# Kernel tuning notes

Measured on AMD Instinct MI355X. Metric: run time of the kernel, lower is better.

The kernel has to match this reference:

```python
import jax, jax.numpy as jnp
from jax import lax
import numpy as np

N = 2000      # num_nodes
T_IN = 24
T_OUT = 12
B = 32
H = 64        # hidden_dim
D = 10        # embed_dim / adapt_dim
K = 2         # cheb_k
C_IN = 1


def setup_inputs() -> dict:
    key = jax.random.key(0)
    ks = jax.random.split(key, 13)
    s = 0.1  # xavier-ish scale
    f32 = jnp.float32
    return {
        "x": jax.random.normal(ks[0], (B, T_IN, N), f32),
        "node_emb": jax.random.normal(ks[1], (N, D), f32) * s,
        "adapt_emb": jax.random.normal(ks[2], (N, D), f32) * s,
        # layer 0 NAPL weight/bias pools (gate: 2H out, candidate: H out)
        "Wg0": jax.random.normal(ks[3], (D, K, C_IN + H, 2 * H), f32) * s,
        "bg0": jax.random.normal(ks[4], (D, 2 * H), f32) * s,
        "Wc0": jax.random.normal(ks[5], (D, K, C_IN + H, H), f32) * s,
        "bc0": jax.random.normal(ks[6], (D, H), f32) * s,
        # layer 1 pools (input is hidden_dim)
        "Wg1": jax.random.normal(ks[7], (D, K, 2 * H, 2 * H), f32) * s,
        "bg1": jax.random.normal(ks[8], (D, 2 * H), f32) * s,
        "Wc1": jax.random.normal(ks[9], (D, K, 2 * H, H), f32) * s,
        "bc1": jax.random.normal(ks[10], (D, H), f32) * s,
        # 1x1 conv head == per-node linear hidden -> T_out
        "head_w": jax.random.normal(ks[11], (T_OUT, H), f32) * s,
        "head_b": jnp.zeros((T_OUT,), f32),
    }


def reference(x, node_emb, adapt_emb, Wg0, bg0, Wc0, bc0, Wg1, bg1, Wc1, bc1,
              head_w, head_b):
    Bn, T, Nn = x.shape
    # adaptive adjacency: row-softmax(relu(E E^T)); no prior -> A_used = A_adapt
    A = jax.nn.softmax(jax.nn.relu(adapt_emb @ adapt_emb.T), axis=-1)
    supports = jnp.stack([jnp.eye(Nn, dtype=x.dtype), A])  # (K, N, N)

    def napl(Wp, bp):
        # node-adaptive parameter learning: per-node weights/biases
        W = jnp.einsum('nd,dkio->nkio', node_emb, Wp)  # (N, K, Cin, Cout)
        b = node_emb @ bp                              # (N, Cout)
        return W, b

    p = [napl(Wg0, bg0), napl(Wc0, bc0), napl(Wg1, bg1), napl(Wc1, bc1)]

    def gconv(inp, W, b):
        # inp: (B, N, C)
        xg = jnp.einsum('knm,bmc->bknc', supports, inp)      # (B, K, N, C)
        return jnp.einsum('bkni,nkio->bno', xg, W) + b       # (B, N, Cout)

    def cell(xt, h, gW, gb, cW, cb):
        zr = jax.nn.sigmoid(gconv(jnp.concatenate([xt, h], -1), gW, gb))
        z, r = jnp.split(zr, 2, axis=-1)
        hc = jnp.tanh(gconv(jnp.concatenate([xt, r * h], -1), cW, cb))
        return z * h + (1.0 - z) * hc

    def step(carry, xt):
        h0, h1 = carry
        h0 = cell(xt, h0, p[0][0], p[0][1], p[1][0], p[1][1])
        h1 = cell(h0, h1, p[2][0], p[2][1], p[3][0], p[3][1])
        return (h0, h1), None

    xs = jnp.transpose(x[..., None], (1, 0, 2, 3))  # (T, B, N, 1)
    h0 = jnp.zeros((Bn, Nn, H), x.dtype)
    h1 = jnp.zeros((Bn, Nn, H), x.dtype)
    (h0, h1), _ = lax.scan(step, (h0, h1), xs)

    # 1x1 conv head on (B, H, N, 1) == per-node linear: (B, T_out, N)
    y = jnp.einsum('bnh,oh->bon', h1, head_w) + head_b[None, :, None]
    return y
```

## Files before the change

### kernel.cpp

```cpp
#include <hip/hip_runtime.h>
#include <math.h>

#define NN 2000
#define BB 32
#define TT 24
#define T_OUT 12
#define HH 64
#define DD 10
#define NP 2048
#define BC 2048

typedef unsigned short ushort_t;
typedef __bf16 bf16x8 __attribute__((ext_vector_type(8)));
typedef float f32x4 __attribute__((ext_vector_type(4)));

__device__ __forceinline__ float sigmoidf_(float x) { return 1.f / (1.f + expf(-x)); }

__device__ __forceinline__ ushort_t f2bf(float f) {
    unsigned int u = __float_as_uint(f);
    unsigned int r = (u + 0x7FFFu + ((u >> 16) & 1u)) >> 16;
    return (ushort_t)r;
}
__device__ __forceinline__ float bf2f(ushort_t s) {
    return __uint_as_float(((unsigned int)s) << 16);
}

__device__ __forceinline__ void glld16(const ushort_t* g, ushort_t* lds) {
    __builtin_amdgcn_global_load_lds(
        (const __attribute__((address_space(1))) char*)g,
        (__attribute__((address_space(3))) char*)lds, 16, 0, 0);
}

__device__ __forceinline__ unsigned lds_off(const void* p) {
    return (unsigned)(size_t)(__attribute__((address_space(3))) const char*)p;
}

constexpr size_t SZ_NPNP2 = (size_t)NP * NP * 2;
constexpr size_t SZ_ST4   = (size_t)NN * BC * 4;
constexpr size_t SZ_NPB2  = (size_t)NP * BC * 2;

constexpr size_t ABF_OFF  = 0;
constexpr size_t H0F_OFF  = ABF_OFF + SZ_NPNP2;
constexpr size_t H1F_OFF  = H0F_OFF + SZ_ST4;
constexpr size_t ZF_OFF   = H1F_OFF + SZ_ST4;
constexpr size_t H0B_OFF  = ZF_OFF + SZ_ST4;
constexpr size_t H1B_OFF  = H0B_OFF + SZ_NPB2;
constexpr size_t RHB_OFF  = H1B_OFF + SZ_NPB2;
constexpr size_t AH0_OFF  = RHB_OFF + SZ_NPB2;
constexpr size_t AHX_OFF  = AH0_OFF + SZ_NPB2;
constexpr size_t AXF_OFF  = AHX_OFF + SZ_NPB2;
constexpr size_t BTG0_OFF = AXF_OFF + (size_t)BB * TT * NN * 4;
constexpr size_t BTC0_OFF = BTG0_OFF + (size_t)DD * 128 * 128 * 2;
constexpr size_t BTG1_OFF = BTC0_OFF + (size_t)DD * 64 * 128 * 2;
constexpr size_t BTC1_OFF = BTG1_OFF + (size_t)DD * 128 * 256 * 2;
constexpr size_t WS_TOP   = BTC1_OFF + (size_t)DD * 64 * 256 * 2;
constexpr size_t ZF1_OFF  = WS_TOP;
constexpr size_t RHB1_OFF = ZF1_OFF + SZ_ST4;
constexpr size_t AHY_OFF  = RHB1_OFF + SZ_NPB2;
constexpr size_t TOP_PIPE = AHY_OFF + SZ_NPB2;
constexpr size_t H0B2_OFF = TOP_PIPE;
constexpr size_t TOP_PIPE2 = H0B2_OFF + SZ_NPB2;

__global__ __launch_bounds__(256) void compute_A_kernel(const float* __restrict__ E,
                                                        float* __restrict__ A) {
    const int row = blockIdx.x;
    const int tid = threadIdx.x;
    float er[DD];
#pragma unroll
    for (int d = 0; d < DD; ++d) er[d] = E[row * DD + d];
    __shared__ float red[8];

    float lmax = -1e30f;
    for (int c = tid; c < NN; c += 256) {
        float s = 0.f;
#pragma unroll
        for (int d = 0; d < DD; ++d) s += er[d] * E[c * DD + d];
        s = fmaxf(s, 0.f);
        A[(size_t)row * NN + c] = s;
        lmax = fmaxf(lmax, s);
    }
#pragma unroll
    for (int o = 32; o > 0; o >>= 1) lmax = fmaxf(lmax, __shfl_down(lmax, o, 64));
    if ((tid & 63) == 0) red[tid >> 6] = lmax;
    __syncthreads();
    const float rmax = fmaxf(fmaxf(red[0], red[1]), fmaxf(red[2], red[3]));
    __syncthreads();

    float lsum = 0.f;
    for (int c = tid; c < NN; c += 256) {
        float v = expf(A[(size_t)row * NN + c] - rmax);
        A[(size_t)row * NN + c] = v;
        lsum += v;
    }
#pragma unroll
    for (int o = 32; o > 0; o >>= 1) lsum += __shfl_down(lsum, o, 64);
    if ((tid & 63) == 0) red[4 + (tid >> 6)] = lsum;
    __syncthreads();
    const float inv = 1.f / (red[4] + red[5] + red[6] + red[7]);
    for (int c = tid; c < NN; c += 256) A[(size_t)row * NN + c] *= inv;
}

__global__ __launch_bounds__(256) void convert_A(const float* __restrict__ Af,
                                                 ushort_t* __restrict__ Ab) {
    size_t idx = (size_t)blockIdx.x * 256 + threadIdx.x;
    int r = (int)(idx >> 11), c = (int)(idx & 2047);
    float v = (r < NN && c < NN) ? Af[(size_t)r * NN + c] : 0.f;
    Ab[idx] = f2bf(v);
}

__global__ __launch_bounds__(256) void ax2_kernel(const float* __restrict__ A,
                                                  const float* __restrict__ x,
                                                  float* __restrict__ Ax) {
    __shared__ float As[64][66];
    __shared__ float xs[64][50];
    const int n0 = blockIdx.x * 64;
    const int b0 = blockIdx.y * 2;
    const int tid = threadIdx.x;
    const int tr = tid >> 4, tc = tid & 15;
    float acc[4][3] = {};

    for (int m0 = 0; m0 < NN; m0 += 64) {
#pragma unroll
        for (int l = 0; l < 16; ++l) {
            int idx = tid + l * 256;
            int mm = idx & 63, r = idx >> 6;
            int n = n0 + r, m = m0 + mm;
            As[mm][r] = (n < NN && m < NN) ? A[(size_t)n * NN + m] : 0.f;
        }
#pragma unroll
        for (int l = 0; l < 12; ++l) {
            int idx = tid + l * 256;
            int mm = idx & 63, col = idx >> 6;
            int m = m0 + mm;
            int bl = col / 24, t = col - bl * 24;
            xs[mm][col] = (m < NN) ? x[((size_t)(b0 + bl) * TT + t) * NN + m] : 0.f;
        }
        __syncthreads();
#pragma unroll 4
        for (int mm = 0; mm < 64; ++mm) {
            float2 a01 = *(const float2*)&As[mm][tr * 4];
            float2 a23 = *(const float2*)&As[mm][tr * 4 + 2];
            float xv[3];
            xv[0] = xs[mm][tc * 3];
            xv[1] = xs[mm][tc * 3 + 1];
            xv[2] = xs[mm][tc * 3 + 2];
            float av[4] = {a01.x, a01.y, a23.x, a23.y};
#pragma unroll
            for (int i = 0; i < 4; ++i)
#pragma unroll
                for (int j = 0; j < 3; ++j) acc[i][j] += av[i] * xv[j];
        }
        __syncthreads();
    }
#pragma unroll
    for (int i = 0; i < 4; ++i) {
        const int n = n0 + tr * 4 + i;
        if (n < NN) {
#pragma unroll
            for (int j = 0; j < 3; ++j) {
                int col = tc * 3 + j;
                int bl = col / 24, t = col - bl * 24;
                Ax[((size_t)(b0 + bl) * TT + t) * NN + n] = acc[i][j];
            }
        }
    }
}


__device__ __forceinline__ void gemm_body(int bx, int by,
                                          const ushort_t* __restrict__ Ab,
                                          const ushort_t* __restrict__ H,
                                          ushort_t* __restrict__ Y, char* smem) {
    ushort_t* As = (ushort_t*)smem;
    ushort_t* Bs = (ushort_t*)(smem + 16384);
    const int tid = threadIdx.x;
    const int w = tid >> 6, l = tid & 63, lr = l & 15, lg = l >> 4;
    const int n0 = bx * 128, j0 = by * 128;
    f32x4 acc[8][2] = {};

    const unsigned bs0 = lds_off(Bs);
    const unsigned btr_b[2] = {
        bs0 + 2u * ((unsigned)(w * 2 + 0) * 512 + (unsigned)lg * 128 + (unsigned)lr),
        bs0 + 2u * ((unsigned)(w * 2 + 1) * 512 + (unsigned)lg * 128 + (unsigned)lr)};

    for (int ks = 0; ks < NP / 64; ++ks) {
        const int k0 = ks * 64;
#pragma unroll
        for (int p = 0; p < 4; ++p) {
            const int idx = p * 256 + tid;
            const int row = idx >> 3, sl = idx & 7;
            glld16(Ab + (size_t)(n0 + row) * NP + k0 + ((sl ^ (row & 7)) << 3),
                   (ushort_t*)((char*)As + idx * 16));
        }
#pragma unroll
        for (int p = 0; p < 4; ++p) {
            const int idx = p * 256 + tid;
            const int g = idx >> 9, li = idx & 511;
            const int row = k0 + g * 32 + ((li >> 3) & 7) * 4 + ((li >> 1) & 3);
            const int col = j0 + (li >> 6) * 16 + (li & 1) * 8;
            glld16(H + (size_t)row * BC + col,
                   (ushort_t*)((char*)Bs + g * 8192 + li * 16));
        }
        __syncthreads();

        unsigned long long bq[2][2][2];
        asm volatile(
            "ds_read_b64_tr_b16 %0, %8 offset:0\n\t"
            "ds_read_b64_tr_b16 %1, %8 offset:128\n\t"
            "ds_read_b64_tr_b16 %2, %9 offset:0\n\t"
            "ds_read_b64_tr_b16 %3, %9 offset:128\n\t"
            "ds_read_b64_tr_b16 %4, %8 offset:8192\n\t"
            "ds_read_b64_tr_b16 %5, %8 offset:8320\n\t"
            "ds_read_b64_tr_b16 %6, %9 offset:8192\n\t"
            "ds_read_b64_tr_b16 %7, %9 offset:8320"
            : "=v"(bq[0][0][0]), "=v"(bq[0][0][1]), "=v"(bq[0][1][0]), "=v"(bq[0][1][1]),
              "=v"(bq[1][0][0]), "=v"(bq[1][0][1]), "=v"(bq[1][1][0]), "=v"(bq[1][1][1])
            : "v"(btr_b[0]), "v"(btr_b[1]));
        asm volatile("s_waitcnt lgkmcnt(0)" ::: "memory");
        __builtin_amdgcn_sched_barrier(0);
        bf16x8 bv[2][2];
#pragma unroll
        for (int kk = 0; kk < 2; ++kk)
#pragma unroll
            for (int nt = 0; nt < 2; ++nt) {
                union { unsigned long long q[2]; bf16x8 f; } u;
                u.q[0] = bq[kk][nt][0];
                u.q[1] = bq[kk][nt][1];
                bv[kk][nt] = u.f;
            }

#pragma unroll
        for (int kk = 0; kk < 2; ++kk)
#pragma unroll
            for (int m = 0; m < 8; ++m) {
                const int rr = m * 16 + lr;
                const bf16x8 av = *(const bf16x8*)&As[rr * 64 + (((kk * 4 + lg) ^ (rr & 7)) << 3)];
#pragma unroll
                for (int nt = 0; nt < 2; ++nt)
                    acc[m][nt] = __builtin_amdgcn_mfma_f32_16x16x32_bf16(av, bv[kk][nt], acc[m][nt], 0, 0, 0);
            }
        __syncthreads();
    }

#pragma unroll
    for (int m = 0; m < 8; ++m)
#pragma unroll
        for (int r = 0; r < 4; ++r) {
            const int n = n0 + m * 16 + lg * 4 + r;
            if (n < NN) {
#pragma unroll
                for (int nt = 0; nt < 2; ++nt)
                    Y[(size_t)n * BC + j0 + w * 32 + nt * 16 + lr] = f2bf(acc[m][nt][r]);
            }
        }
}

template <int NSEGS, int CO, bool GATE, bool HASX>
__device__ __forceinline__ void napl_body(
    int bid, char* smem,
    const ushort_t* __restrict__ Bt, const float* __restrict__ bp,
    const float* __restrict__ emb, const float* __restrict__ WxPool,
    const ushort_t* __restrict__ s0p, const ushort_t* __restrict__ s1p,
    const ushort_t* __restrict__ s2p, const ushort_t* __restrict__ s3p,
    const float* __restrict__ xv, const float* __restrict__ axv,
    const float* hf, float* __restrict__ zf,
    ushort_t* __restrict__ outb, float* outf, int t) {
    constexpr int K = NSEGS * 64;
    constexpr int NT = (CO == 128) ? 2 : 1;
    constexpr int NHALF = NSEGS / 2;
    ushort_t* As = (ushort_t*)smem;
    const int tid = threadIdx.x;
    const int w = tid >> 6, l = tid & 63, lr = l & 15, lg = l >> 4;
    const int n0 = bid * 2;
    const int ob = w * (16 * NT);
    const ushort_t* segs[4] = {s0p, s1p, s2p, s3p};

#pragma unroll
    for (int s = 0; s < NSEGS; ++s) {
        const ushort_t* sp = segs[s];
#pragma unroll
        for (int p = 0; p < 2; ++p) {
            const int idx = p * 256 + tid;
            const int row = idx >> 3, c16 = idx & 7;
            glld16(sp + (size_t)(n0 + (row >> 5)) * BC + (row & 31) * 64 +
                       ((c16 ^ (row & 7)) << 3),
                   (ushort_t*)((char*)As + s * 8192 + idx * 16));
        }
    }
    __syncthreads();

    f32x4 OUT[4][NT] = {};
#pragma unroll 1
    for (int hf2 = 0; hf2 < NHALF; ++hf2) {
        bf16x8 av[4][4];
#pragma unroll
        for (int c = 0; c < 4; ++c) {
            const int s = hf2 * 2 + (c >> 1);
            const int kin = (c & 1) * 32 + lg * 8;
#pragma unroll
            for (int m = 0; m < 4; ++m) {
                const int rr = m * 16 + lr;
                av[c][m] = *(const bf16x8*)&As[s * 4096 + rr * 64 + (kin ^ ((rr & 7) << 3))];
            }
        }
#pragma unroll 1
        for (int d = 0; d < DD; ++d) {
            const ushort_t* btd = Bt + (size_t)d * CO * K;
            const float ea = emb[n0 * DD + d];
            const float eb = emb[(n0 + 1) * DD + d];
            f32x4 P[4][NT] = {};
#pragma unroll
            for (int c = 0; c < 4; ++c) {
                const int kg = (hf2 * 2 + (c >> 1)) * 64 + (c & 1) * 32 + lg * 8;
                bf16x8 bv[NT];
#pragma unroll
                for (int nt = 0; nt < NT; ++nt)
                    bv[nt] = *(const bf16x8*)&btd[(size_t)(ob + nt * 16 + lr) * K + kg];
#pragma unroll
                for (int m = 0; m < 4; ++m)
#pragma unroll
                    for (int nt = 0; nt < NT; ++nt)
                        P[m][nt] = __builtin_amdgcn_mfma_f32_16x16x32_bf16(av[c][m], bv[nt], P[m][nt], 0, 0, 0);
            }
#pragma unroll
            for (int m = 0; m < 4; ++m) {
                const float e = (m < 2) ? ea : eb;
#pragma unroll
                for (int nt = 0; nt < NT; ++nt)
#pragma unroll
                    for (int r = 0; r < 4; ++r)
                        OUT[m][nt][r] += e * P[m][nt][r];
            }
        }
    }

    float bias[2][NT];
#pragma unroll
    for (int nd = 0; nd < 2; ++nd)
#pragma unroll
        for (int nt = 0; nt < NT; ++nt) {
            float s_ = 0.f;
#pragma unroll
            for (int d = 0; d < DD; ++d)
                s_ += emb[(n0 + nd) * DD + d] * bp[d * CO + ob + nt * 16 + lr];
            bias[nd][nt] = s_;
        }
    float wx[2][2][NT] = {};
    if (HASX) {
#pragma unroll
        for (int kk = 0; kk < 2; ++kk)
#pragma unroll
            for (int nd = 0; nd < 2; ++nd)
#pragma unroll
                for (int nt = 0; nt < NT; ++nt) {
                    float s_ = 0.f;
#pragma unroll
                    for (int d = 0; d < DD; ++d)
                        s_ += emb[(n0 + nd) * DD + d] *
                              WxPool[(size_t)(d * 2 + kk) * 65 * CO + ob + nt * 16 + lr];
                    wx[kk][nd][nt] = s_;
                }
    }

#pragma unroll
    for (int m = 0; m < 4; ++m) {
        const int nd = m >> 1;
        const int n = n0 + nd;
#pragma unroll
        for (int r = 0; r < 4; ++r) {
            const int row = m * 16 + lg * 4 + r;
            const int b = row & 31;
            const size_t nb = (size_t)n * BC + b * 64;
            float xt = 0.f, axt = 0.f;
            if (HASX) {
                xt = xv[((size_t)b * TT + t) * NN + n];
                axt = axv[((size_t)b * TT + t) * NN + n];
            }
#pragma unroll
            for (int nt = 0; nt < NT; ++nt) {
                const int o = ob + nt * 16 + lr;
                float val = OUT[m][nt][r] + bias[nd][nt];
                if (HASX) val += xt * wx[0][nd][nt] + axt * wx[1][nd][nt];
                if (GATE) {
                    const float sg = sigmoidf_(val);
                    if (ob < 64) {
                        zf[nb + o] = sg;
                    } else {
                        outb[nb + (o - 64)] = f2bf(sg * hf[nb + (o - 64)]);
                    }
                } else {
                    const float hc = tanhf(val);
                    const float z = zf[nb + o];
                    const float hn = z * hf[nb + o] + (1.f - z) * hc;
                    outf[nb + o] = hn;
                    outb[nb + o] = f2bf(hn);
                }
            }
        }
    }
}


__global__ __launch_bounds__(256) void gemm_trb(const ushort_t* __restrict__ Ab,
                                                const ushort_t* __restrict__ H0,
                                                ushort_t* __restrict__ Y0,
                                                const ushort_t* __restrict__ H1,
                                                ushort_t* __restrict__ Y1) {
    __shared__ __align__(16) char smem[32768];
    gemm_body(blockIdx.x, blockIdx.y, Ab,
              (blockIdx.z == 0) ? H0 : H1, (blockIdx.z == 0) ? Y0 : Y1, smem);
}

template <int NSEGS, int CO, bool GATE, bool HASX>
__global__ __launch_bounds__(256) void napl2(
    const ushort_t* __restrict__ Bt, const float* __restrict__ bp,
    const float* __restrict__ emb, const float* __restrict__ WxPool,
    const ushort_t* __restrict__ s0p, const ushort_t* __restrict__ s1p,
    const ushort_t* __restrict__ s2p, const ushort_t* __restrict__ s3p,
    const float* __restrict__ xv, const float* __restrict__ axv,
    const float* hf, float* __restrict__ zf,
    ushort_t* __restrict__ outb, float* outf, int t) {
    __shared__ __align__(16) char smem[NSEGS * 8192];
    napl_body<NSEGS, CO, GATE, HASX>(blockIdx.x, smem, Bt, bp, emb, WxPool,
                                     s0p, s1p, s2p, s3p, xv, axv, hf, zf, outb, outf, t);
}

__global__ __launch_bounds__(256) void mergeA_k(
    const ushort_t* __restrict__ Abf, const ushort_t* __restrict__ Hg,
    ushort_t* __restrict__ Yg,
    const ushort_t* __restrict__ Bt, const float* __restrict__ bp,
    const float* __restrict__ emb, const float* __restrict__ Wx,
    const ushort_t* __restrict__ s0, const ushort_t* __restrict__ s1,
    const float* __restrict__ xv, const float* __restrict__ axv,
    const float* hf, float* __restrict__ zf, ushort_t* __restrict__ outb, int t) {
    __shared__ __align__(16) char smem[32768];
    const int g = blockIdx.x;
    if (g < 256)
        gemm_body(g & 15, g >> 4, Abf, Hg, Yg, smem);
    else
        napl_body<2, 128, true, true>(g - 256, smem, Bt, bp, emb, Wx,
                                      s0, s1, s0, s0, xv, axv, hf, zf, outb, nullptr, t);
}

__global__ __launch_bounds__(256) void mergeB_k(
    const ushort_t* __restrict__ Abf, const ushort_t* __restrict__ Hg,
    ushort_t* __restrict__ Yg,
    const ushort_t* __restrict__ Bt, const float* __restrict__ bp,
    const float* __restrict__ emb,
    const ushort_t* __restrict__ s0, const ushort_t* __restrict__ s1,
    const ushort_t* __restrict__ s2, const ushort_t* __restrict__ s3,
    const float* hf, float* __restrict__ zf,
    ushort_t* __restrict__ outb, float* outf, int t) {
    __shared__ __align__(16) char smem[32768];
    const int g = blockIdx.x;
    if (g < 256)
        gemm_body(g & 15, g >> 4, Abf, Hg, Yg, smem);
    else
        napl_body<4, 64, false, false>(g - 256, smem, Bt, bp, emb, nullptr,
                                       s0, s1, s2, s3, nullptr, nullptr, hf, zf, outb, outf, t);
}

__global__ __launch_bounds__(256) void mergeC_k(
    const ushort_t* __restrict__ Abf, const ushort_t* __restrict__ Hg,
    ushort_t* __restrict__ Yg,
    const ushort_t* __restrict__ Bt, const float* __restrict__ bp,
    const float* __restrict__ emb, const float* __restrict__ Wx,
    const ushort_t* __restrict__ s0, const ushort_t* __restrict__ s1,
    const float* __restrict__ xv, const float* __restrict__ axv,
    const float* hf, float* __restrict__ zf,
    ushort_t* __restrict__ outb, float* outf, int t) {
    __shared__ __align__(16) char smem[32768];
    const int g = blockIdx.x;
    if (g < 256)
        gemm_body(g & 15, g >> 4, Abf, Hg, Yg, smem);
    else
        napl_body<2, 64, false, true>(g - 256, smem, Bt, bp, emb, Wx,
                                      s0, s1, s0, s0, xv, axv, hf, zf, outb, outf, t);
}

__global__ __launch_bounds__(256) void mergeG_k(
    const ushort_t* __restrict__ Btg1, const float* __restrict__ bg1,
    const ushort_t* __restrict__ Btg0, const float* __restrict__ bg0,
    const float* __restrict__ emb, const float* __restrict__ Wg0,
    const ushort_t* __restrict__ hbt, const ushort_t* __restrict__ Ah0,
    const ushort_t* __restrict__ h1b, const ushort_t* __restrict__ AhX,
    const float* __restrict__ xv, const float* __restrict__ axv,
    const float* h0f, const float* h1f,
    float* __restrict__ zf0, float* __restrict__ zf1,
    ushort_t* __restrict__ rhb0, ushort_t* __restrict__ rhb1, int t) {
    __shared__ __align__(16) char smem[32768];
    const int g = blockIdx.x;
    if (g < 1000)
        napl_body<4, 128, true, false>(g, smem, Btg1, bg1, emb, nullptr,
                                       hbt, Ah0, h1b, AhX, nullptr, nullptr,
                                       h1f, zf1, rhb1, nullptr, t);
    else
        napl_body<2, 128, true, true>(g - 1000, smem, Btg0, bg0, emb, Wg0,
                                      hbt, Ah0, hbt, hbt, xv, axv,
                                      h0f, zf0, rhb0, nullptr, t + 1);
}

__global__ __launch_bounds__(256) void mergeCC_k(
    const ushort_t* __restrict__ Btc1, const float* __restrict__ bc1,
    const ushort_t* __restrict__ Btc0, const float* __restrict__ bc0,
    const float* __restrict__ emb, const float* __restrict__ Wc0,
    const ushort_t* __restrict__ hbt, ushort_t* __restrict__ hbt1,
    const ushort_t* __restrict__ Ah0, const ushort_t* __restrict__ rhb1,
    const ushort_t* __restrict__ AhX, const ushort_t* __restrict__ AhY,
    const ushort_t* __restrict__ rhb0,
    const float* __restrict__ xv, const float* __restrict__ axv,
    float* h0f, float* h1f,
    float* __restrict__ zf0, float* __restrict__ zf1,
    ushort_t* __restrict__ h1b, int t) {
    __shared__ __align__(16) char smem[32768];
    const int g = blockIdx.x;
    if (g < 1000)
        napl_body<4, 64, false, false>(g, smem, Btc1, bc1, emb, nullptr,
                                       hbt, Ah0, rhb1, AhX, nullptr, nullptr,
                                       h1f, zf1, h1b, h1f, t);
    else
        napl_body<2, 64, false, true>(g - 1000, smem, Btc0, bc0, emb, Wc0,
                                      rhb0, AhY, rhb0, rhb0, xv, axv,
                                      h0f, zf0, hbt1, h0f, t + 1);
}

template <int CI, int CO, bool L0>
__global__ __launch_bounds__(256) void prepW(const float* __restrict__ Wp,
                                             ushort_t* __restrict__ Bt) {
    constexpr int K = L0 ? 128 : 256;
    const int idx = blockIdx.x * 256 + threadIdx.x;
    if (idx >= DD * CO * K) return;
    const int d = idx / (CO * K);
    const int rem = idx - d * CO * K;
    const int o = rem / K;
    const int k = rem - o * K;
    const int s = k >> 6, c = k & 63;
    const int kk = L0 ? s : (s & 1);
    const int i = L0 ? (1 + c) : ((s >> 1) * 64 + c);
    Bt[idx] = f2bf(Wp[((size_t)(d * 2 + kk) * CI + i) * CO + o]);
}

__global__ __launch_bounds__(256) void head_kernel(const float* __restrict__ h1,
                                                   const float* __restrict__ hw,
                                                   const float* __restrict__ hb,
                                                   float* __restrict__ y) {
    __shared__ float wl[T_OUT * HH];
    const int tid = threadIdx.x;
    for (int idx = tid; idx < T_OUT * HH; idx += 256) wl[idx] = hw[idx];
    __syncthreads();
    const int gi = blockIdx.x * 256 + tid;
    if (gi >= BB * NN) return;
    const int b = gi / NN, n = gi % NN;
    float acc[T_OUT];
#pragma unroll
    for (int ot = 0; ot < T_OUT; ++ot) acc[ot] = hb[ot];
    for (int h = 0; h < HH; ++h) {
        float v = h1[(size_t)n * BC + b * 64 + h];
#pragma unroll
        for (int ot = 0; ot < T_OUT; ++ot) acc[ot] += v * wl[ot * HH + h];
    }
#pragma unroll
    for (int ot = 0; ot < T_OUT; ++ot)
        y[((size_t)b * T_OUT + ot) * NN + n] = acc[ot];
}

extern "C" void kernel_launch(void* const* d_in, const int* in_sizes, int n_in,
                              void* d_out, int out_size, void* d_ws, size_t ws_size,
                              hipStream_t stream) {
    const float* x = (const float*)d_in[0];
    const float* node_emb = (const float*)d_in[1];
    const float* adapt_emb = (const float*)d_in[2];
    const float* Wg0 = (const float*)d_in[3];
    const float* bg0 = (const float*)d_in[4];
    const float* Wc0 = (const float*)d_in[5];
    const float* bc0 = (const float*)d_in[6];
    const float* Wg1 = (const float*)d_in[7];
    const float* bg1 = (const float*)d_in[8];
    const float* Wc1 = (const float*)d_in[9];
    const float* bc1 = (const float*)d_in[10];
    const float* head_w = (const float*)d_in[11];
    const float* head_b = (const float*)d_in[12];
    float* y = (float*)d_out;

    char* ws = (char*)d_ws;
    ushort_t* Abf  = (ushort_t*)(ws + ABF_OFF);
    float* h0f = (float*)(ws + H0F_OFF);
    float* h1f = (float*)(ws + H1F_OFF);
    float* zf  = (float*)(ws + ZF_OFF);
    ushort_t* h0b = (ushort_t*)(ws + H0B_OFF);
    ushort_t* h1b = (ushort_t*)(ws + H1B_OFF);
    ushort_t* rhb = (ushort_t*)(ws + RHB_OFF);
    ushort_t* Ah0 = (ushort_t*)(ws + AH0_OFF);
    ushort_t* AhX = (ushort_t*)(ws + AHX_OFF);
    float* Axf = (float*)(ws + AXF_OFF);
    ushort_t* Btg0 = (ushort_t*)(ws + BTG0_OFF);
    ushort_t* Btc0 = (ushort_t*)(ws + BTC0_OFF);
    ushort_t* Btg1 = (ushort_t*)(ws + BTG1_OFF);
    ushort_t* Btc1 = (ushort_t*)(ws + BTC1_OFF);
    float* Af32 = zf;

    const bool pipe2 = (ws_size >= TOP_PIPE2);
    const bool pipe = (ws_size >= TOP_PIPE);

    hipMemsetAsync(h0f, 0, SZ_ST4, stream);
    hipMemsetAsync(h1f, 0, SZ_ST4, stream);
    hipMemsetAsync(h0b, 0, SZ_NPB2, stream);
    hipMemsetAsync(h1b, 0, SZ_NPB2, stream);
    hipMemsetAsync(rhb, 0, SZ_NPB2, stream);
    hipMemsetAsync(Ah0, 0, SZ_NPB2, stream);
    hipMemsetAsync(AhX, 0, SZ_NPB2, stream);

    compute_A_kernel<<<NN, 256, 0, stream>>>(adapt_emb, Af32);
    ax2_kernel<<<dim3(32, 16), 256, 0, stream>>>(Af32, x, Axf);
    convert_A<<<(NP * NP) / 256, 256, 0, stream>>>(Af32, Abf);
    prepW<65, 128, true><<<(DD * 128 * 128 + 255) / 256, 256, 0, stream>>>(Wg0, Btg0);
    prepW<65, 64, true><<<(DD * 64 * 128 + 255) / 256, 256, 0, stream>>>(Wc0, Btc0);
    prepW<128, 128, false><<<(DD * 128 * 256 + 255) / 256, 256, 0, stream>>>(Wg1, Btg1);
    prepW<128, 64, false><<<(DD * 64 * 256 + 255) / 256, 256, 0, stream>>>(Wc1, Btc1);

    const dim3 gG1(NP / 128, NP / 128, 1);
    const dim3 gG2(NP / 128, NP / 128, 2);
    const int gN = NN * BB / 64;

    if (pipe2) {
        float* zf0 = zf;
        ushort_t* rhb0 = rhb;
        float* zf1 = (float*)(ws + ZF1_OFF);
        ushort_t* rhb1 = (ushort_t*)(ws + RHB1_OFF);
        ushort_t* AhY = (ushort_t*)(ws + AHY_OFF);
        ushort_t* h0b2 = (ushort_t*)(ws + H0B2_OFF);
        hipMemsetAsync(rhb1, 0, SZ_NPB2, stream);
        hipMemsetAsync(h0b2, 0, SZ_NPB2, stream);
        ushort_t* hb[2] = {h0b, h0b2};

        napl2<2, 128, true, true><<<gN, 256, 0, stream>>>(
            Btg0, bg0, node_emb, Wg0, h0b, Ah0, h0b, h0b, x, Axf, h0f, zf0, rhb0, nullptr, 0);
        gemm_trb<<<gG1, 256, 0, stream>>>(Abf, rhb0, AhY, rhb0, AhY);
        napl2<2, 64, false, true><<<gN, 256, 0, stream>>>(
            Btc0, bc0, node_emb, Wc0, rhb0, AhY, rhb0, rhb0, x, Axf, h0f, zf0, hb[0], h0f, 0);
        gemm_trb<<<gG1, 256, 0, stream>>>(Abf, hb[0], Ah0, hb[0], Ah0);

        for (int t = 0; t < TT - 1; ++t) {
            ushort_t* hbt = hb[t & 1];
            ushort_t* hbt1 = hb[(t + 1) & 1];
            mergeG_k<<<2000, 256, 0, stream>>>(Btg1, bg1, Btg0, bg0, node_emb, Wg0,
                hbt, Ah0, h1b, AhX, x, Axf, h0f, h1f, zf0, zf1, rhb0, rhb1, t);
            gemm_trb<<<gG2, 256, 0, stream>>>(Abf, rhb1, AhX, rhb0, AhY);
            mergeCC_k<<<2000, 256, 0, stream>>>(Btc1, bc1, Btc0, bc0, node_emb, Wc0,
                hbt, hbt1, Ah0, rhb1, AhX, AhY, rhb0, x, Axf, h0f, h1f, zf0, zf1, h1b, t);
            gemm_trb<<<gG2, 256, 0, stream>>>(Abf, h1b, AhX, hbt1, Ah0);
        }
        {
            ushort_t* hbT = hb[(TT - 1) & 1];
            napl2<4, 128, true, false><<<gN, 256, 0, stream>>>(
                Btg1, bg1, node_emb, nullptr, hbT, Ah0, h1b, AhX, nullptr, nullptr, h1f, zf1, rhb1, nullptr, TT - 1);
            gemm_trb<<<gG1, 256, 0, stream>>>(Abf, rhb1, AhX, rhb1, AhX);
            napl2<4, 64, false, false><<<gN, 256, 0, stream>>>(
                Btc1, bc1, node_emb, nullptr, hbT, Ah0, rhb1, AhX, nullptr, nullptr, h1f, zf1, h1b, h1f, TT - 1);
        }
    } else if (pipe) {
        float* zf0 = zf;
        ushort_t* rhb0 = rhb;
        float* zf1 = (float*)(ws + ZF1_OFF);
        ushort_t* rhb1 = (ushort_t*)(ws + RHB1_OFF);
        ushort_t* AhY = (ushort_t*)(ws + AHY_OFF);
        hipMemsetAsync(rhb1, 0, SZ_NPB2, stream);

        napl2<2, 128, true, true><<<gN, 256, 0, stream>>>(
            Btg0, bg0, node_emb, Wg0, h0b, Ah0, h0b, h0b, x, Axf, h0f, zf0, rhb0, nullptr, 0);
        gemm_trb<<<gG1, 256, 0, stream>>>(Abf, rhb0, AhY, rhb0, AhY);
        napl2<2, 64, false, true><<<gN, 256, 0, stream>>>(
            Btc0, bc0, node_emb, Wc0, rhb0, AhY, rhb0, rhb0, x, Axf, h0f, zf0, h0b, h0f, 0);
        gemm_trb<<<gG2, 256, 0, stream>>>(Abf, h0b, Ah0, h1b, AhX);
        napl2<4, 128, true, false><<<gN, 256, 0, stream>>>(
            Btg1, bg1, node_emb, nullptr, h0b, Ah0, h1b, AhX, nullptr, nullptr, h1f, zf1, rhb1, nullptr, 0);

        for (int t = 0; t < TT - 1; ++t) {
            mergeA_k<<<1256, 256, 0, stream>>>(Abf, rhb1, AhX,
                Btg0, bg0, node_emb, Wg0, h0b, Ah0, x, Axf, h0f, zf0, rhb0, t + 1);
            mergeB_k<<<1256, 256, 0, stream>>>(Abf, rhb0, AhY,
                Btc1, bc1, node_emb, h0b, Ah0, rhb1, AhX, h1f, zf1, h1b, h1f, t);
            mergeC_k<<<1256, 256, 0, stream>>>(Abf, h1b, AhX,
                Btc0, bc0, node_emb, Wc0, rhb0, AhY, x, Axf, h0f, zf0, h0b, h0f, t + 1);
            gemm_trb<<<gG1, 256, 0, stream>>>(Abf, h0b, Ah0, h0b, Ah0);
            napl2<4, 128, true, false><<<gN, 256, 0, stream>>>(
                Btg1, bg1, node_emb, nullptr, h0b, Ah0, h1b, AhX, nullptr, nullptr, h1f, zf1, rhb1, nullptr, t + 1);
        }
        gemm_trb<<<gG1, 256, 0, stream>>>(Abf, rhb1, AhX, rhb1, AhX);
        napl2<4, 64, false, false><<<gN, 256, 0, stream>>>(
            Btc1, bc1, node_emb, nullptr, h0b, Ah0, rhb1, AhX, nullptr, nullptr, h1f, zf1, h1b, h1f, TT - 1);
    } else {
        for (int t = 0; t < TT; ++t) {
            napl2<2, 128, true, true><<<gN, 256, 0, stream>>>(
                Btg0, bg0, node_emb, Wg0, h0b, Ah0, h0b, h0b, x, Axf, h0f, zf, rhb, nullptr, t);
            gemm_trb<<<gG1, 256, 0, stream>>>(Abf, rhb, AhX, rhb, AhX);
            napl2<2, 64, false, true><<<gN, 256, 0, stream>>>(
                Btc0, bc0, node_emb, Wc0, rhb, AhX, rhb, rhb, x, Axf, h0f, zf, h0b, h0f, t);
            gemm_trb<<<gG2, 256, 0, stream>>>(Abf, h0b, Ah0, h1b, AhX);
            napl2<4, 128, true, false><<<gN, 256, 0, stream>>>(
                Btg1, bg1, node_emb, nullptr, h0b, Ah0, h1b, AhX, nullptr, nullptr, h1f, zf, rhb, nullptr, t);
            gemm_trb<<<gG1, 256, 0, stream>>>(Abf, rhb, AhX, rhb, AhX);
            napl2<4, 64, false, false><<<gN, 256, 0, stream>>>(
                Btc1, bc1, node_emb, nullptr, h0b, Ah0, rhb, AhX, nullptr, nullptr, h1f, zf, h1b, h1f, t);
        }
    }

    head_kernel<<<(BB * NN + 255) / 256, 256, 0, stream>>>(h1f, head_w, head_b, y);
}
```

Measured before the change: 8.223 ms.

## Use 8-wave blocks for standalone A·H GEMM and retile ax2 per batch

The standalone gemm_trb GEMM now runs 512 threads (8 waves), each wave owning one 16-column strip instead of two. This halves per-wave accumulators and B-fragment loads and spreads the global-to-LDS loads across more threads, aiming for better latency hiding. The merged kernels keep the 4-wave variant through a template parameter. Separately, the one-time A·x precompute is retiled to one batch per block with one node per lane, doubling its grid. Both trade per-thread register reuse for more parallelism, and the 8-wave GEMM may see more barrier contention.

Result: no change. 8.110 ms (-1.4%).

```diff
diff --git a/kernel.cpp b/kernel.cpp
--- a/kernel.cpp
+++ b/kernel.cpp
@@ -112,12 +112,12 @@
                                                   const float* __restrict__ x,
                                                   float* __restrict__ Ax) {
     __shared__ float As[64][66];
-    __shared__ float xs[64][50];
+    __shared__ float xs[64][26];
     const int n0 = blockIdx.x * 64;
-    const int b0 = blockIdx.y * 2;
+    const int b = blockIdx.y;
     const int tid = threadIdx.x;
-    const int tr = tid >> 4, tc = tid & 15;
-    float acc[4][3] = {};
+    const int lane = tid & 63, cq = tid >> 6;
+    float acc[6] = {};
 
     for (int m0 = 0; m0 < NN; m0 += 64) {
 #pragma unroll
@@ -128,73 +128,71 @@
             As[mm][r] = (n < NN && m < NN) ? A[(size_t)n * NN + m] : 0.f;
         }
 #pragma unroll
-        for (int l = 0; l < 12; ++l) {
+        for (int l = 0; l < 6; ++l) {
             int idx = tid + l * 256;
-            int mm = idx & 63, col = idx >> 6;
+            int mm = idx & 63, t = idx >> 6;
             int m = m0 + mm;
-            int bl = col / 24, t = col - bl * 24;
-            xs[mm][col] = (m < NN) ? x[((size_t)(b0 + bl) * TT + t) * NN + m] : 0.f;
+            xs[mm][t] = (m < NN) ? x[((size_t)b * TT + t) * NN + m] : 0.f;
         }
         __syncthreads();
 #pragma unroll 4
         for (int mm = 0; mm < 64; ++mm) {
-            float2 a01 = *(const float2*)&As[mm][tr * 4];
-            float2 a23 = *(const float2*)&As[mm][tr * 4 + 2];
-            float xv[3];
-            xv[0] = xs[mm][tc * 3];
-            xv[1] = xs[mm][tc * 3 + 1];
-            xv[2] = xs[mm][tc * 3 + 2];
-            float av[4] = {a01.x, a01.y, a23.x, a23.y};
-#pragma unroll
-            for (int i = 0; i < 4; ++i)
-#pragma unroll
-                for (int j = 0; j < 3; ++j) acc[i][j] += av[i] * xv[j];
+            const float a = As[mm][lane];
+            float2 x01 = *(const float2*)&xs[mm][cq * 6];
+            float2 x23 = *(const float2*)&xs[mm][cq * 6 + 2];
+            float2 x45 = *(const float2*)&xs[mm][cq * 6 + 4];
+            acc[0] += a * x01.x;
+            acc[1] += a * x01.y;
+            acc[2] += a * x23.x;
+            acc[3] += a * x23.y;
+            acc[4] += a * x45.x;
+            acc[5] += a * x45.y;
         }
         __syncthreads();
     }
-#pragma unroll
-    for (int i = 0; i < 4; ++i) {
-        const int n = n0 + tr * 4 + i;
-        if (n < NN) {
-#pragma unroll
-            for (int j = 0; j < 3; ++j) {
-                int col = tc * 3 + j;
-                int bl = col / 24, t = col - bl * 24;
-                Ax[((size_t)(b0 + bl) * TT + t) * NN + n] = acc[i][j];
-            }
-        }
-    }
-}
-
-
+    const int n = n0 + lane;
+    if (n < NN) {
+#pragma unroll
+        for (int j = 0; j < 6; ++j) {
+            const int t = cq * 6 + j;
+            Ax[((size_t)b * TT + t) * NN + n] = acc[j];
+        }
+    }
+}
+
+
+template <int NW>
 __device__ __forceinline__ void gemm_body(int bx, int by,
                                           const ushort_t* __restrict__ Ab,
                                           const ushort_t* __restrict__ H,
                                           ushort_t* __restrict__ Y, char* smem) {
+    constexpr int TH = NW * 64;
+    constexpr int SPW = 8 / NW;
     ushort_t* As = (ushort_t*)smem;
     ushort_t* Bs = (ushort_t*)(smem + 16384);
     const int tid = threadIdx.x;
     const int w = tid >> 6, l = tid & 63, lr = l & 15, lg = l >> 4;
     const int n0 = bx * 128, j0 = by * 128;
-    f32x4 acc[8][2] = {};
+    f32x4 acc[8][SPW] = {};
 
     const unsigned bs0 = lds_off(Bs);
-    const unsigned btr_b[2] = {
-        bs0 + 2u * ((unsigned)(w * 2 + 0) * 512 + (unsigned)lg * 128 + (unsigned)lr),
-        bs0 + 2u * ((unsigned)(w * 2 + 1) * 512 + (unsigned)lg * 128 + (unsigned)lr)};
+    unsigned btr_b[SPW];
+#pragma unroll
+    for (int nt = 0; nt < SPW; ++nt)
+        btr_b[nt] = bs0 + 2u * ((unsigned)(w * SPW + nt) * 512 + (unsigned)lg * 128 + (unsigned)lr);
 
     for (int ks = 0; ks < NP / 64; ++ks) {
         const int k0 = ks * 64;
 #pragma unroll
-        for (int p = 0; p < 4; ++p) {
-            const int idx = p * 256 + tid;
+        for (int p = 0; p < 1024 / TH; ++p) {
+            const int idx = p * TH + tid;
             const int row = idx >> 3, sl = idx & 7;
             glld16(Ab + (size_t)(n0 + row) * NP + k0 + ((sl ^ (row & 7)) << 3),
                    (ushort_t*)((char*)As + idx * 16));
         }
 #pragma unroll
-        for (int p = 0; p < 4; ++p) {
-            const int idx = p * 256 + tid;
+        for (int p = 0; p < 1024 / TH; ++p) {
+            const int idx = p * TH + tid;
             const int g = idx >> 9, li = idx & 511;
             const int row = k0 + g * 32 + ((li >> 3) & 7) * 4 + ((li >> 1) & 3);
             const int col = j0 + (li >> 6) * 16 + (li & 1) * 8;
@@ -203,26 +201,36 @@
         }
         __syncthreads();
 
-        unsigned long long bq[2][2][2];
-        asm volatile(
-            "ds_read_b64_tr_b16 %0, %8 offset:0\n\t"
-            "ds_read_b64_tr_b16 %1, %8 offset:128\n\t"
-            "ds_read_b64_tr_b16 %2, %9 offset:0\n\t"
-            "ds_read_b64_tr_b16 %3, %9 offset:128\n\t"
-            "ds_read_b64_tr_b16 %4, %8 offset:8192\n\t"
-            "ds_read_b64_tr_b16 %5, %8 offset:8320\n\t"
-            "ds_read_b64_tr_b16 %6, %9 offset:8192\n\t"
-            "ds_read_b64_tr_b16 %7, %9 offset:8320"
-            : "=v"(bq[0][0][0]), "=v"(bq[0][0][1]), "=v"(bq[0][1][0]), "=v"(bq[0][1][1]),
-              "=v"(bq[1][0][0]), "=v"(bq[1][0][1]), "=v"(bq[1][1][0]), "=v"(bq[1][1][1])
-            : "v"(btr_b[0]), "v"(btr_b[1]));
+        unsigned long long bq[2][SPW][2];
+        if constexpr (SPW == 2) {
+            asm volatile(
+                "ds_read_b64_tr_b16 %0, %8 offset:0\n\t"
+                "ds_read_b64_tr_b16 %1, %8 offset:128\n\t"
+                "ds_read_b64_tr_b16 %2, %9 offset:0\n\t"
+                "ds_read_b64_tr_b16 %3, %9 offset:128\n\t"
+                "ds_read_b64_tr_b16 %4, %8 offset:8192\n\t"
+                "ds_read_b64_tr_b16 %5, %8 offset:8320\n\t"
+                "ds_read_b64_tr_b16 %6, %9 offset:8192\n\t"
+                "ds_read_b64_tr_b16 %7, %9 offset:8320"
+                : "=v"(bq[0][0][0]), "=v"(bq[0][0][1]), "=v"(bq[0][1][0]), "=v"(bq[0][1][1]),
+                  "=v"(bq[1][0][0]), "=v"(bq[1][0][1]), "=v"(bq[1][1][0]), "=v"(bq[1][1][1])
+                : "v"(btr_b[0]), "v"(btr_b[1]));
+        } else {
+            asm volatile(
+                "ds_read_b64_tr_b16 %0, %4 offset:0\n\t"
+                "ds_read_b64_tr_b16 %1, %4 offset:128\n\t"
+                "ds_read_b64_tr_b16 %2, %4 offset:8192\n\t"
+                "ds_read_b64_tr_b16 %3, %4 offset:8320"
+                : "=v"(bq[0][0][0]), "=v"(bq[0][0][1]), "=v"(bq[1][0][0]), "=v"(bq[1][0][1])
+                : "v"(btr_b[0]));
+        }
         asm volatile("s_waitcnt lgkmcnt(0)" ::: "memory");
         __builtin_amdgcn_sched_barrier(0);
-        bf16x8 bv[2][2];
+        bf16x8 bv[2][SPW];
 #pragma unroll
         for (int kk = 0; kk < 2; ++kk)
 #pragma unroll
-            for (int nt = 0; nt < 2; ++nt) {
+            for (int nt = 0; nt < SPW; ++nt) {
                 union { unsigned long long q[2]; bf16x8 f; } u;
                 u.q[0] = bq[kk][nt][0];
                 u.q[1] = bq[kk][nt][1];
@@ -236,7 +244,7 @@
                 const int rr = m * 16 + lr;
                 const bf16x8 av = *(const bf16x8*)&As[rr * 64 + (((kk * 4 + lg) ^ (rr & 7)) << 3)];
 #pragma unroll
-                for (int nt = 0; nt < 2; ++nt)
+                for (int nt = 0; nt < SPW; ++nt)
                     acc[m][nt] = __builtin_amdgcn_mfma_f32_16x16x32_bf16(av, bv[kk][nt], acc[m][nt], 0, 0, 0);
             }
         __syncthreads();
@@ -249,8 +257,8 @@
             const int n = n0 + m * 16 + lg * 4 + r;
             if (n < NN) {
 #pragma unroll
-                for (int nt = 0; nt < 2; ++nt)
-                    Y[(size_t)n * BC + j0 + w * 32 + nt * 16 + lr] = f2bf(acc[m][nt][r]);
+                for (int nt = 0; nt < SPW; ++nt)
+                    Y[(size_t)n * BC + j0 + (w * SPW + nt) * 16 + lr] = f2bf(acc[m][nt][r]);
             }
         }
 }
@@ -401,14 +409,14 @@
 }
 
 
-__global__ __launch_bounds__(256) void gemm_trb(const ushort_t* __restrict__ Ab,
+__global__ __launch_bounds__(512) void gemm_trb(const ushort_t* __restrict__ Ab,
                                                 const ushort_t* __restrict__ H0,
                                                 ushort_t* __restrict__ Y0,
                                                 const ushort_t* __restrict__ H1,
                                                 ushort_t* __restrict__ Y1) {
     __shared__ __align__(16) char smem[32768];
-    gemm_body(blockIdx.x, blockIdx.y, Ab,
-              (blockIdx.z == 0) ? H0 : H1, (blockIdx.z == 0) ? Y0 : Y1, smem);
+    gemm_body<8>(blockIdx.x, blockIdx.y, Ab,
+                 (blockIdx.z == 0) ? H0 : H1, (blockIdx.z == 0) ? Y0 : Y1, smem);
 }
 
 template <int NSEGS, int CO, bool GATE, bool HASX>
@@ -436,7 +444,7 @@
     __shared__ __align__(16) char smem[32768];
     const int g = blockIdx.x;
     if (g < 256)
-        gemm_body(g & 15, g >> 4, Abf, Hg, Yg, smem);
+        gemm_body<4>(g & 15, g >> 4, Abf, Hg, Yg, smem);
     else
         napl_body<2, 128, true, true>(g - 256, smem, Bt, bp, emb, Wx,
                                       s0, s1, s0, s0, xv, axv, hf, zf, outb, nullptr, t);
@@ -454,7 +462,7 @@
     __shared__ __align__(16) char smem[32768];
     const int g = blockIdx.x;
     if (g < 256)
-        gemm_body(g & 15, g >> 4, Abf, Hg, Yg, smem);
+        gemm_body<4>(g & 15, g >> 4, Abf, Hg, Yg, smem);
     else
         napl_body<4, 64, false, false>(g - 256, smem, Bt, bp, emb, nullptr,
                                        s0, s1, s2, s3, nullptr, nullptr, hf, zf, outb, outf, t);
@@ -472,7 +480,7 @@
     __shared__ __align__(16) char smem[32768];
     const int g = blockIdx.x;
     if (g < 256)
-        gemm_body(g & 15, g >> 4, Abf, Hg, Yg, smem);
+        gemm_body<4>(g & 15, g >> 4, Abf, Hg, Yg, smem);
     else
         napl_body<2, 64, false, true>(g - 256, smem, Bt, bp, emb, Wx,
                                       s0, s1, s0, s0, xv, axv, hf, zf, outb, outf, t);
@@ -611,7 +619,7 @@
     hipMemsetAsync(AhX, 0, SZ_NPB2, stream);
 
     compute_A_kernel<<<NN, 256, 0, stream>>>(adapt_emb, Af32);
-    ax2_kernel<<<dim3(32, 16), 256, 0, stream>>>(Af32, x, Axf);
+    ax2_kernel<<<dim3(32, 32), 256, 0, stream>>>(Af32, x, Axf);
     convert_A<<<(NP * NP) / 256, 256, 0, stream>>>(Af32, Abf);
     prepW<65, 128, true><<<(DD * 128 * 128 + 255) / 256, 256, 0, stream>>>(Wg0, Btg0);
     prepW<65, 64, true><<<(DD * 64 * 128 + 255) / 256, 256, 0, stream>>>(Wc0, Btc0);
@@ -635,26 +643,26 @@
 
         napl2<2, 128, true, true><<<gN, 256, 0, stream>>>(
             Btg0, bg0, node_emb, Wg0, h0b, Ah0, h0b, h0b, x, Axf, h0f, zf0, rhb0, nullptr, 0);
-        gemm_trb<<<gG1, 256, 0, stream>>>(Abf, rhb0, AhY, rhb0, AhY);
+        gemm_trb<<<gG1, 512, 0, stream>>>(Abf, rhb0, AhY, rhb0, AhY);
         napl2<2, 64, false, true><<<gN, 256, 0, stream>>>(
             Btc0, bc0, node_emb, Wc0, rhb0, AhY, rhb0, rhb0, x, Axf, h0f, zf0, hb[0], h0f, 0);
-        gemm_trb<<<gG1, 256, 0, stream>>>(Abf, hb[0], Ah0, hb[0], Ah0);
+        gemm_trb<<<gG1, 512, 0, stream>>>(Abf, hb[0], Ah0, hb[0], Ah0);
 
         for (int t = 0; t < TT - 1; ++t) {
             ushort_t* hbt = hb[t & 1];
             ushort_t* hbt1 = hb[(t + 1) & 1];
             mergeG_k<<<2000, 256, 0, stream>>>(Btg1, bg1, Btg0, bg0, node_emb, Wg0,
                 hbt, Ah0, h1b, AhX, x, Axf, h0f, h1f, zf0, zf1, rhb0, rhb1, t);
-            gemm_trb<<<gG2, 256, 0, stream>>>(Abf, rhb1, AhX, rhb0, AhY);
+            gemm_trb<<<gG2, 512, 0, stream>>>(Abf, rhb1, AhX, rhb0, AhY);
             mergeCC_k<<<2000, 256, 0, stream>>>(Btc1, bc1, Btc0, bc0, node_emb, Wc0,
                 hbt, hbt1, Ah0, rhb1, AhX, AhY, rhb0, x, Axf, h0f, h1f, zf0, zf1, h1b, t);
-            gemm_trb<<<gG2, 256, 0, stream>>>(Abf, h1b, AhX, hbt1, Ah0);
+            gemm_trb<<<gG2, 512, 0, stream>>>(Abf, h1b, AhX, hbt1, Ah0);
         }
         {
             ushort_t* hbT = hb[(TT - 1) & 1];
             napl2<4, 128, true, false><<<gN, 256, 0, stream>>>(
                 Btg1, bg1, node_emb, nullptr, hbT, Ah0, h1b, AhX, nullptr, nullptr, h1f, zf1, rhb1, nullptr, TT - 1);
-            gemm_trb<<<gG1, 256, 0, stream>>>(Abf, rhb1, AhX, rhb1, AhX);
+            gemm_trb<<<gG1, 512, 0, stream>>>(Abf, rhb1, AhX, rhb1, AhX);
             napl2<4, 64, false, false><<<gN, 256, 0, stream>>>(
                 Btc1, bc1, node_emb, nullptr, hbT, Ah0, rhb1, AhX, nullptr, nullptr, h1f, zf1, h1b, h1f, TT - 1);
         }
@@ -668,10 +676,10 @@
 
         napl2<2, 128, true, true><<<gN, 256, 0, stream>>>(
             Btg0, bg0, node_emb, Wg0, h0b, Ah0, h0b, h0b, x, Axf, h0f, zf0, rhb0, nullptr, 0);
-        gemm_trb<<<gG1, 256, 0, stream>>>(Abf, rhb0, AhY, rhb0, AhY);
+        gemm_trb<<<gG1, 512, 0, stream>>>(Abf, rhb0, AhY, rhb0, AhY);
         napl2<2, 64, false, true><<<gN, 256, 0, stream>>>(
             Btc0, bc0, node_emb, Wc0, rhb0, AhY, rhb0, rhb0, x, Axf, h0f, zf0, h0b, h0f, 0);
-        gemm_trb<<<gG2, 256, 0, stream>>>(Abf, h0b, Ah0, h1b, AhX);
+        gemm_trb<<<gG2, 512, 0, stream>>>(Abf, h0b, Ah0, h1b, AhX);
         napl2<4, 128, true, false><<<gN, 256, 0, stream>>>(
             Btg1, bg1, node_emb, nullptr, h0b, Ah0, h1b, AhX, nullptr, nullptr, h1f, zf1, rhb1, nullptr, 0);
 
@@ -682,24 +690,24 @@
                 Btc1, bc1, node_emb, h0b, Ah0, rhb1, AhX, h1f, zf1, h1b, h1f, t);
             mergeC_k<<<1256, 256, 0, stream>>>(Abf, h1b, AhX,
                 Btc0, bc0, node_emb, Wc0, rhb0, AhY, x, Axf, h0f, zf0, h0b, h0f, t + 1);
-            gemm_trb<<<gG1, 256, 0, stream>>>(Abf, h0b, Ah0, h0b, Ah0);
+            gemm_trb<<<gG1, 512, 0, stream>>>(Abf, h0b, Ah0, h0b, Ah0);
             napl2<4, 128, true, false><<<gN, 256, 0, stream>>>(
                 Btg1, bg1, node_emb, nullptr, h0b, Ah0, h1b, AhX, nullptr, nullptr, h1f, zf1, rhb1, nullptr, t + 1);
         }
-        gemm_trb<<<gG1, 256, 0, stream>>>(Abf, rhb1, AhX, rhb1, AhX);
+        gemm_trb<<<gG1, 512, 0, stream>>>(Abf, rhb1, AhX, rhb1, AhX);
         napl2<4, 64, false, false><<<gN, 256, 0, stream>>>(
             Btc1, bc1, node_emb, nullptr, h0b, Ah0, rhb1, AhX, nullptr, nullptr, h1f, zf1, h1b, h1f, TT - 1);
     } else {
         for (int t = 0; t < TT; ++t) {
             napl2<2, 128, true, true><<<gN, 256, 0, stream>>>(
                 Btg0, bg0, node_emb, Wg0, h0b, Ah0, h0b, h0b, x, Axf, h0f, zf, rhb, nullptr, t);
-            gemm_trb<<<gG1, 256, 0, stream>>>(Abf, rhb, AhX, rhb, AhX);
+            gemm_trb<<<gG1, 512, 0, stream>>>(Abf, rhb, AhX, rhb, AhX);
             napl2<2, 64, false, true><<<gN, 256, 0, stream>>>(
                 Btc0, bc0, node_emb, Wc0, rhb, AhX, rhb, rhb, x, Axf, h0f, zf, h0b, h0f, t);
-            gemm_trb<<<gG2, 256, 0, stream>>>(Abf, h0b, Ah0, h1b, AhX);
+            gemm_trb<<<gG2, 512, 0, stream>>>(Abf, h0b, Ah0, h1b, AhX);
             napl2<4, 128, true, false><<<gN, 256, 0, stream>>>(
                 Btg1, bg1, node_emb, nullptr, h0b, Ah0, h1b, AhX, nullptr, nullptr, h1f, zf, rhb, nullptr, t);
-            gemm_trb<<<gG1, 256, 0, stream>>>(Abf, rhb, AhX, rhb, AhX);
+            gemm_trb<<<gG1, 512, 0, stream>>>(Abf, rhb, AhX, rhb, AhX);
             napl2<4, 64, false, false><<<gN, 256, 0, stream>>>(
                 Btc1, bc1, node_emb, nullptr, h0b, Ah0, rhb, AhX, nullptr, nullptr, h1f, zf, h1b, h1f, t);
         }
```
